# Optimization experiments

Hardware: AMD Instinct MI355X
Metric: run time of the kernel (lower is better)

Reference implementation:

```python
import jax, jax.numpy as jnp
import numpy as np

H = 16
D_MODEL = 1024
D_K = D_MODEL // H


def setup_inputs() -> dict:
    key = jax.random.key(0)
    ks = jax.random.split(key, 11)
    B, S, D = 2, 2048, D_MODEL
    sc = 1.0 / np.sqrt(D)
    return {
        "query": jax.random.normal(ks[0], (B, S, D), jnp.float32),
        "key": jax.random.normal(ks[1], (B, S, D), jnp.float32),
        "value": jax.random.normal(ks[2], (B, S, D), jnp.float32),
        "Wq": jax.random.normal(ks[3], (D, D), jnp.float32) * sc,
        "bq": jnp.zeros((D,), jnp.float32),
        "Wk": jax.random.normal(ks[4], (D, D), jnp.float32) * sc,
        "bk": jnp.zeros((D,), jnp.float32),
        "Wv": jax.random.normal(ks[5], (D, D), jnp.float32) * sc,
        "bv": jnp.zeros((D,), jnp.float32),
        "Wo": jax.random.normal(ks[6], (D, D), jnp.float32) * sc,
        "bo": jnp.zeros((D,), jnp.float32),
    }


def _split_heads(x, B, S):
    # [B,S,D] -> [B,H,S,d_k]
    return x.reshape(B, S, H, D_K).transpose(0, 2, 1, 3)


def reference(query, key, value, Wq, bq, Wk, bk, Wv, bv, Wo, bo):
    B, S, D = query.shape
    q = _split_heads(query @ Wq + bq, B, S)
    k = _split_heads(key @ Wk + bk, B, key.shape[1])
    v = _split_heads(value @ Wv + bv, B, value.shape[1])
    scores = jnp.einsum("bhqd,bhkd->bhqk", q, k) / jnp.sqrt(jnp.asarray(D_K, q.dtype))
    p_attn = jax.nn.softmax(scores, axis=-1)  # dropout is identity at inference
    x = jnp.einsum("bhqk,bhkd->bhqd", p_attn, v)
    x = x.transpose(0, 2, 1, 3).reshape(B, S, H * D_K)
    return x @ Wo + bo
```

## Files before the change

### kernel.cpp

```cpp
#include <hip/hip_runtime.h>

typedef unsigned short u16;
typedef unsigned int   u32;
typedef __bf16 bf16x8 __attribute__((ext_vector_type(8)));
typedef float  f32x4  __attribute__((ext_vector_type(4)));

__device__ __forceinline__ u16 f2bf(float f) {
  u32 u = __float_as_uint(f);
  u += 0x7fffu + ((u >> 16) & 1u);
  return (u16)(u >> 16);
}

__device__ __forceinline__ u32 cvt_pk_bf16(float a, float b) {
  u32 r;
  asm("v_cvt_pk_bf16_f32 %0, %1, %2" : "=v"(r) : "v"(a), "v"(b));
  return r;
}

__device__ __forceinline__ float max3f(float a, float b, float c) {
  float r;
  asm("v_max3_f32 %0, %1, %2, %3" : "=v"(r) : "v"(a), "v"(b), "v"(c));
  return r;
}

__device__ __forceinline__ void gll16(const void* g, void* l) {
  __builtin_amdgcn_global_load_lds(
      (__attribute__((address_space(1))) unsigned int*)(g),
      (__attribute__((address_space(3))) unsigned int*)(l), 16, 0, 0);
}

__device__ __forceinline__ int xcd_swz(int wg, int nwg) {
  int cpx = nwg >> 3;
  return (wg & 7) * cpx + (wg >> 3);
}

__device__ __forceinline__ void cvt8(const float* __restrict__ s, u16* __restrict__ d, int o) {
  float4 a = *(const float4*)(s + o);
  float4 b = *(const float4*)(s + o + 4);
  uint4 r;
  r.x = cvt_pk_bf16(a.x, a.y);
  r.y = cvt_pk_bf16(a.z, a.w);
  r.z = cvt_pk_bf16(b.x, b.y);
  r.w = cvt_pk_bf16(b.z, b.w);
  *(uint4*)(d + o) = r;
}

__global__ __launch_bounds__(256) void convert_in(
    const float* __restrict__ q, const float* __restrict__ k, const float* __restrict__ v,
    u16* __restrict__ qo, u16* __restrict__ ko, u16* __restrict__ vo) {
  int t = blockIdx.x * 256 + threadIdx.x;
  int o = t * 8;
  cvt8(q, qo, o);
  cvt8(k, ko, o);
  cvt8(v, vo, o);
}

__global__ __launch_bounds__(256) void convert_w(
    const float* __restrict__ Wq, const float* __restrict__ Wk,
    const float* __restrict__ Wv, const float* __restrict__ Wo,
    u16* __restrict__ Wqt, u16* __restrict__ Wkt,
    u16* __restrict__ Wvt, u16* __restrict__ Wot) {
  __shared__ __align__(16) u16 t[64][72];
  int z = blockIdx.z;
  const float* W = (z == 0) ? Wq : (z == 1) ? Wk : (z == 2) ? Wv : Wo;
  u16* Wt = (z == 0) ? Wqt : (z == 1) ? Wkt : (z == 2) ? Wvt : Wot;
  int k0 = blockIdx.y * 64, n0 = blockIdx.x * 64;
  int tid = threadIdx.x;
#pragma unroll
  for (int e = 0; e < 4; ++e) {
    int i = e * 256 + tid;
    int r = i >> 4, c4 = (i & 15) * 4;
    float4 vv = *(const float4*)(W + (size_t)(k0 + r) * 1024 + n0 + c4);
    union { u16 u[4]; uint2 w2; } p;
    p.u[0] = f2bf(vv.x); p.u[1] = f2bf(vv.y); p.u[2] = f2bf(vv.z); p.u[3] = f2bf(vv.w);
    *(uint2*)&t[r][c4] = p.w2;
  }
  __syncthreads();
#pragma unroll
  for (int e = 0; e < 2; ++e) {
    int i = e * 256 + tid;
    int rn = i >> 3, c8 = (i & 7) * 8;
    union { u16 u[8]; uint4 w4; } p;
#pragma unroll
    for (int kk = 0; kk < 8; ++kk) p.u[kk] = t[c8 + kk][rn];
    *(uint4*)(Wt + (size_t)(n0 + rn) * 1024 + k0 + c8) = p.w4;
  }
}

__device__ __forceinline__ void gemm_core(
    const u16* __restrict__ A,
    const u16* __restrict__ Bt,
    int K, int m0, int n0,
    u16* As, u16* Bs, f32x4 acc[4][4]) {
  const int tid = threadIdx.x;
  const int l = tid & 63;
  const int g = l >> 4, q16 = l & 15;
  const int wv = tid >> 6;
  const int wr = wv >> 1, wc = wv & 1;
#pragma unroll
  for (int mi = 0; mi < 4; ++mi)
#pragma unroll
    for (int ni = 0; ni < 4; ++ni) acc[mi][ni] = (f32x4){0.f, 0.f, 0.f, 0.f};

  for (int k0 = 0; k0 < K; k0 += 64) {
    __syncthreads();
#pragma unroll
    for (int c = 0; c < 4; ++c) {
      int i = c * 256 + tid;
      int row = i >> 3, ce = (i & 7) * 8;
      gll16(A + (size_t)(m0 + row) * K + k0 + ce, As + i * 8);
      gll16(Bt + (size_t)(n0 + row) * K + k0 + ce, Bs + i * 8);
    }
    __syncthreads();
#pragma unroll
    for (int kb = 0; kb < 2; ++kb) {
      bf16x8 af[4], bfr[4];
#pragma unroll
      for (int mi = 0; mi < 4; ++mi)
        af[mi] = *(const bf16x8*)(As + (wr * 64 + mi * 16 + q16) * 64 + kb * 32 + g * 8);
#pragma unroll
      for (int ni = 0; ni < 4; ++ni)
        bfr[ni] = *(const bf16x8*)(Bs + (wc * 64 + ni * 16 + q16) * 64 + kb * 32 + g * 8);
#pragma unroll
      for (int mi = 0; mi < 4; ++mi)
#pragma unroll
        for (int ni = 0; ni < 4; ++ni)
          acc[mi][ni] = __builtin_amdgcn_mfma_f32_16x16x32_bf16(af[mi], bfr[ni], acc[mi][ni], 0, 0, 0);
    }
  }
}

__global__ __launch_bounds__(256) void gemm_qkv(
    const u16* __restrict__ qA, const u16* __restrict__ kA, const u16* __restrict__ vA,
    const u16* __restrict__ qW, const u16* __restrict__ kW, const u16* __restrict__ vW,
    const float* __restrict__ qb, const float* __restrict__ kb2, const float* __restrict__ vb,
    u16* __restrict__ Qh, u16* __restrict__ Kh, u16* __restrict__ Vh, float qscale) {
  __shared__ __align__(16) u16 As[128 * 64];
  __shared__ __align__(16) u16 Bs[128 * 64];
  int z = blockIdx.z;
  const u16* A   = (z == 0) ? qA : (z == 1) ? kA : vA;
  const u16* Bt  = (z == 0) ? qW : (z == 1) ? kW : vW;
  const float* bias = (z == 0) ? qb : (z == 1) ? kb2 : vb;
  u16* out = (z == 0) ? Qh : (z == 1) ? Kh : Vh;
  float scale = (z == 0) ? qscale : 1.0f;
  int swz = xcd_swz(blockIdx.y * gridDim.x + blockIdx.x, gridDim.x * gridDim.y);
  int m0 = (swz >> 3) * 128, n0 = (swz & 7) * 128;
  f32x4 acc[4][4];
  gemm_core(A, Bt, 1024, m0, n0, As, Bs, acc);

  const int tid = threadIdx.x;
  const int l = tid & 63;
  const int g = l >> 4, q16 = l & 15;
  const int wv = tid >> 6;
  const int wr = wv >> 1, wc = wv & 1;
#pragma unroll
  for (int ni = 0; ni < 4; ++ni) {
    int n = n0 + wc * 64 + ni * 16 + q16;
    float bvv = bias[n];
    int hh = n >> 6, dk = n & 63;
#pragma unroll
    for (int mi = 0; mi < 4; ++mi) {
#pragma unroll
      for (int j = 0; j < 4; ++j) {
        int m = m0 + wr * 64 + mi * 16 + g * 4 + j;
        int b = m >> 11, s = m & 2047;
        float v = (acc[mi][ni][j] + bvv) * scale;
        out[(((size_t)b * 16 + hh) * 2048 + s) * 64 + dk] = f2bf(v);
      }
    }
  }
}

__global__ __launch_bounds__(256) void gemm_out(
    const u16* __restrict__ A, const u16* __restrict__ Bt,
    const float* __restrict__ bias, float* __restrict__ Out) {
  __shared__ __align__(16) u16 As[128 * 64];
  __shared__ __align__(16) u16 Bs[128 * 64];
  int swz = xcd_swz(blockIdx.y * gridDim.x + blockIdx.x, gridDim.x * gridDim.y);
  int m0 = (swz >> 3) * 128, n0 = (swz & 7) * 128;
  f32x4 acc[4][4];
  gemm_core(A, Bt, 1024, m0, n0, As, Bs, acc);

  const int tid = threadIdx.x;
  const int l = tid & 63;
  const int g = l >> 4, q16 = l & 15;
  const int wv = tid >> 6;
  const int wr = wv >> 1, wc = wv & 1;
#pragma unroll
  for (int ni = 0; ni < 4; ++ni) {
    int n = n0 + wc * 64 + ni * 16 + q16;
    float bvv = bias[n];
#pragma unroll
    for (int mi = 0; mi < 4; ++mi) {
#pragma unroll
      for (int j = 0; j < 4; ++j) {
        int m = m0 + wr * 64 + mi * 16 + g * 4 + j;
        Out[(size_t)m * 1024 + n] = acc[mi][ni][j] + bvv;
      }
    }
  }
}

__global__ __launch_bounds__(256) void transpose_v(const u16* __restrict__ Vh, u16* __restrict__ Vt) {
  __shared__ __align__(16) u16 t[64][72];
  int bh = blockIdx.y, s0 = blockIdx.x * 64;
  int tid = threadIdx.x;
#pragma unroll
  for (int e = 0; e < 2; ++e) {
    int i = e * 256 + tid;
    int r = i >> 3, c8 = (i & 7) * 8;
    uint4 vv = *(const uint4*)(Vh + ((size_t)bh * 2048 + s0 + r) * 64 + c8);
    *(uint4*)&t[r][c8] = vv;
  }
  __syncthreads();
#pragma unroll
  for (int e = 0; e < 2; ++e) {
    int i = e * 256 + tid;
    int d = i >> 3, s8 = (i & 7) * 8;
    union { u16 u[8]; uint4 w4; } p;
#pragma unroll
    for (int kk = 0; kk < 8; ++kk) p.u[kk] = t[s8 + kk][d];
    *(uint4*)(Vt + ((size_t)bh * 64 + d) * 2048 + s0 + s8) = p.w4;
  }
}

__global__ __launch_bounds__(256, 3) void attn_kernel(
    const u16* __restrict__ Qh,
    const u16* __restrict__ Kh,
    const u16* __restrict__ Vt,
    u16* __restrict__ Xb) {
  __shared__ __align__(16) u16 Ks[2][64 * 64];
  __shared__ __align__(16) u16 Vs[2][64 * 64];
  __shared__ __align__(16) u16 Ps[4][16][72];

  const int tid = threadIdx.x;
  const int l = tid & 63, wv = tid >> 6;
  const int g = l >> 4, q16 = l & 15;
  int swz = xcd_swz(blockIdx.y * gridDim.x + blockIdx.x, gridDim.x * gridDim.y);
  const int qblk = swz & 31, bh = swz >> 5;
  const int b = bh >> 4, h = bh & 15;
  const int qrow0 = qblk * 64 + wv * 16;

  const u16* Kbase = Kh + (size_t)bh * 2048 * 64;
  const u16* Vbase = Vt + (size_t)bh * 64 * 2048;

  bf16x8 bq[2];
#pragma unroll
  for (int kb = 0; kb < 2; ++kb)
    bq[kb] = *(const bf16x8*)(Qh + ((size_t)bh * 2048 + qrow0 + q16) * 64 + kb * 32 + g * 8);

  f32x4 x[4];
#pragma unroll
  for (int ni = 0; ni < 4; ++ni) x[ni] = (f32x4){0.f, 0.f, 0.f, 0.f};
  float m_run = -3e38f, l_run = 0.f;

#pragma unroll
  for (int c = 0; c < 2; ++c) {
    int i = c * 256 + tid;
    int row = i >> 3, sc8 = (i & 7) ^ (row & 7);
    gll16(Kbase + (size_t)row * 64 + sc8 * 8, &Ks[0][i * 8]);
    gll16(Vbase + (size_t)row * 2048 + sc8 * 8, &Vs[0][i * 8]);
  }
  asm volatile("s_waitcnt vmcnt(0)" ::: "memory");
  __builtin_amdgcn_s_barrier();

  for (int kt = 0; kt < 32; ++kt) {
    const int cb = kt & 1, nb = cb ^ 1;
    if (kt + 1 < 32) {
#pragma unroll
      for (int c = 0; c < 2; ++c) {
        int i = c * 256 + tid;
        int row = i >> 3, sc8 = (i & 7) ^ (row & 7);
        gll16(Kbase + ((size_t)(kt + 1) * 64 + row) * 64 + sc8 * 8, &Ks[nb][i * 8]);
        gll16(Vbase + (size_t)row * 2048 + (kt + 1) * 64 + sc8 * 8, &Vs[nb][i * 8]);
      }
    }

    f32x4 st[4];
#pragma unroll
    for (int mi = 0; mi < 4; ++mi) st[mi] = (f32x4){0.f, 0.f, 0.f, 0.f};
    __builtin_amdgcn_s_setprio(1);
#pragma unroll
    for (int mi = 0; mi < 4; ++mi) {
      int row = mi * 16 + q16;
#pragma unroll
      for (int kb = 0; kb < 2; ++kb) {
        int pc8 = (kb * 4 + g) ^ (row & 7);
        bf16x8 ak = *(const bf16x8*)(&Ks[cb][row * 64 + pc8 * 8]);
        st[mi] = __builtin_amdgcn_mfma_f32_16x16x32_bf16(ak, bq[kb], st[mi], 0, 0, 0);
      }
    }
    __builtin_amdgcn_s_setprio(0);

    float ma = max3f(st[0][0], st[0][1], st[0][2]);
    ma = max3f(ma, st[0][3], st[1][0]);
    ma = max3f(ma, st[1][1], st[1][2]);
    ma = fmaxf(ma, st[1][3]);
    float mb = max3f(st[2][0], st[2][1], st[2][2]);
    mb = max3f(mb, st[2][3], st[3][0]);
    mb = max3f(mb, st[3][1], st[3][2]);
    mb = fmaxf(mb, st[3][3]);
    float mx = fmaxf(ma, mb);
    mx = fmaxf(mx, __shfl_xor(mx, 16));
    mx = fmaxf(mx, __shfl_xor(mx, 32));

    float mref, sf;
    if (__all(mx <= m_run + 8.f)) {
      mref = m_run; sf = 1.f;
    } else {
      mref = fmaxf(m_run, mx);
      sf = __builtin_amdgcn_exp2f(m_run - mref);
      m_run = mref;
#pragma unroll
      for (int j = 0; j < 4; ++j) {
        float sfx = __shfl(sf, g * 4 + j);
#pragma unroll
        for (int ni = 0; ni < 4; ++ni) x[ni][j] *= sfx;
      }
    }

    float rs = 0.f;
#pragma unroll
    for (int mi = 0; mi < 4; ++mi)
#pragma unroll
      for (int j = 0; j < 4; ++j) {
        float p = __builtin_amdgcn_exp2f(st[mi][j] - mref);
        st[mi][j] = p;
        rs += p;
      }
    rs += __shfl_xor(rs, 16);
    rs += __shfl_xor(rs, 32);
    l_run = l_run * sf + rs;

#pragma unroll
    for (int mi = 0; mi < 4; ++mi) {
      uint2 w;
      w.x = cvt_pk_bf16(st[mi][0], st[mi][1]);
      w.y = cvt_pk_bf16(st[mi][2], st[mi][3]);
      *(uint2*)&Ps[wv][q16][mi * 16 + g * 4] = w;
    }

    __builtin_amdgcn_s_setprio(1);
#pragma unroll
    for (int kkb = 0; kkb < 2; ++kkb) {
      bf16x8 ap = *(const bf16x8*)&Ps[wv][q16][kkb * 32 + g * 8];
#pragma unroll
      for (int ni = 0; ni < 4; ++ni) {
        int d = ni * 16 + q16;
        int pc8 = (kkb * 4 + g) ^ (d & 7);
        bf16x8 vf = *(const bf16x8*)(&Vs[cb][d * 64 + pc8 * 8]);
        x[ni] = __builtin_amdgcn_mfma_f32_16x16x32_bf16(ap, vf, x[ni], 0, 0, 0);
      }
    }
    __builtin_amdgcn_s_setprio(0);

    asm volatile("s_waitcnt vmcnt(0)" ::: "memory");
    __builtin_amdgcn_s_barrier();
  }

  float li = 1.0f / l_run;
#pragma unroll
  for (int j = 0; j < 4; ++j) {
    float lv = __shfl(li, g * 4 + j);
    int srw = b * 2048 + qblk * 64 + wv * 16 + g * 4 + j;
#pragma unroll
    for (int ni = 0; ni < 4; ++ni) {
      int col = h * 64 + ni * 16 + q16;
      Xb[(size_t)srw * 1024 + col] = f2bf(x[ni][j] * lv);
    }
  }
}

extern "C" void kernel_launch(void* const* d_in, const int* in_sizes, int n_in,
                              void* d_out, int out_size, void* d_ws, size_t ws_size,
                              hipStream_t stream) {
  (void)in_sizes; (void)n_in; (void)out_size; (void)ws_size;
  const float* q  = (const float*)d_in[0];
  const float* k  = (const float*)d_in[1];
  const float* v  = (const float*)d_in[2];
  const float* Wq = (const float*)d_in[3];
  const float* bq = (const float*)d_in[4];
  const float* Wk = (const float*)d_in[5];
  const float* bk = (const float*)d_in[6];
  const float* Wv = (const float*)d_in[7];
  const float* bv = (const float*)d_in[8];
  const float* Wo = (const float*)d_in[9];
  const float* bo = (const float*)d_in[10];

  char* W = (char*)d_ws;
  const size_t MB = 1ull << 20;
  u16* qbf = (u16*)(W + 0 * MB);
  u16* kbf = (u16*)(W + 8 * MB);
  u16* vbf = (u16*)(W + 16 * MB);
  u16* wqt = (u16*)(W + 24 * MB);
  u16* wkt = (u16*)(W + 26 * MB);
  u16* wvt = (u16*)(W + 28 * MB);
  u16* wot = (u16*)(W + 30 * MB);
  u16* Qh  = (u16*)(W + 32 * MB);
  u16* Kh  = (u16*)(W + 40 * MB);
  u16* Vh  = (u16*)(W + 48 * MB);
  u16* Vtb = (u16*)(W + 56 * MB);
  u16* Xb  = (u16*)(W + 64 * MB);

  convert_in<<<2048, 256, 0, stream>>>(q, k, v, qbf, kbf, vbf);
  convert_w<<<dim3(16, 16, 4), 256, 0, stream>>>(Wq, Wk, Wv, Wo, wqt, wkt, wvt, wot);
  const float QSCALE = 0.125f * 1.4426950408889634f;
  gemm_qkv<<<dim3(8, 32, 3), 256, 0, stream>>>(qbf, kbf, vbf, wqt, wkt, wvt,
                                               bq, bk, bv, Qh, Kh, Vh, QSCALE);
  transpose_v<<<dim3(32, 32), 256, 0, stream>>>(Vh, Vtb);
  attn_kernel<<<dim3(32, 32), 256, 0, stream>>>(Qh, Kh, Vtb, Xb);
  gemm_out<<<dim3(8, 32), 256, 0, stream>>>(Xb, wot, bo, (float*)d_out);
}
```

Before: 177.9 us.

## Use 128-query attention blocks with 8 waves and triple-buffered K/V prefetch

The attention kernel now uses 512-thread blocks, each covering 128 query rows with 8 waves, so every K/V tile loaded into shared memory serves twice as many queries. K/V staging moves from double to triple buffering with a two-tile-ahead prefetch and a partial vmcnt wait, so loads overlap more compute. The s_setprio hints around the MFMA sections are removed. The costs are a grid of half as many blocks, more shared memory per block, and lower occupancy control, since the launch bound changes from (256,3) to (512).

```diff
diff --git a/kernel.cpp b/kernel.cpp
--- a/kernel.cpp
+++ b/kernel.cpp
@@ -224,23 +224,25 @@
   }
 }
 
-__global__ __launch_bounds__(256, 3) void attn_kernel(
+__global__ __launch_bounds__(512) void attn_kernel(
     const u16* __restrict__ Qh,
     const u16* __restrict__ Kh,
     const u16* __restrict__ Vt,
     u16* __restrict__ Xb) {
-  __shared__ __align__(16) u16 Ks[2][64 * 64];
-  __shared__ __align__(16) u16 Vs[2][64 * 64];
-  __shared__ __align__(16) u16 Ps[4][16][72];
+  __shared__ __align__(16) u16 Ks[3][64 * 64];
+  __shared__ __align__(16) u16 Vs[3][64 * 64];
+  __shared__ __align__(16) u16 Ps[8][16][72];
 
   const int tid = threadIdx.x;
   const int l = tid & 63, wv = tid >> 6;
   const int g = l >> 4, q16 = l & 15;
-  int swz = xcd_swz(blockIdx.y * gridDim.x + blockIdx.x, gridDim.x * gridDim.y);
-  const int qblk = swz & 31, bh = swz >> 5;
+  const int swz = xcd_swz(blockIdx.y * gridDim.x + blockIdx.x, gridDim.x * gridDim.y);
+  const int qblk = swz & 15, bh = swz >> 4;
   const int b = bh >> 4, h = bh & 15;
-  const int qrow0 = qblk * 64 + wv * 16;
-
+  const int qrow0 = qblk * 128 + wv * 16;
+
+  const int srow = tid >> 3;
+  const int sc8  = (tid & 7) ^ (srow & 7);
   const u16* Kbase = Kh + (size_t)bh * 2048 * 64;
   const u16* Vbase = Vt + (size_t)bh * 64 * 2048;
 
@@ -254,32 +256,24 @@
   for (int ni = 0; ni < 4; ++ni) x[ni] = (f32x4){0.f, 0.f, 0.f, 0.f};
   float m_run = -3e38f, l_run = 0.f;
 
-#pragma unroll
-  for (int c = 0; c < 2; ++c) {
-    int i = c * 256 + tid;
-    int row = i >> 3, sc8 = (i & 7) ^ (row & 7);
-    gll16(Kbase + (size_t)row * 64 + sc8 * 8, &Ks[0][i * 8]);
-    gll16(Vbase + (size_t)row * 2048 + sc8 * 8, &Vs[0][i * 8]);
-  }
-  asm volatile("s_waitcnt vmcnt(0)" ::: "memory");
+  gll16(Kbase + (size_t)srow * 64 + sc8 * 8, &Ks[0][tid * 8]);
+  gll16(Vbase + (size_t)srow * 2048 + sc8 * 8, &Vs[0][tid * 8]);
+  gll16(Kbase + ((size_t)64 + srow) * 64 + sc8 * 8, &Ks[1][tid * 8]);
+  gll16(Vbase + (size_t)srow * 2048 + 64 + sc8 * 8, &Vs[1][tid * 8]);
+  asm volatile("s_waitcnt vmcnt(2)" ::: "memory");
   __builtin_amdgcn_s_barrier();
 
   for (int kt = 0; kt < 32; ++kt) {
-    const int cb = kt & 1, nb = cb ^ 1;
-    if (kt + 1 < 32) {
-#pragma unroll
-      for (int c = 0; c < 2; ++c) {
-        int i = c * 256 + tid;
-        int row = i >> 3, sc8 = (i & 7) ^ (row & 7);
-        gll16(Kbase + ((size_t)(kt + 1) * 64 + row) * 64 + sc8 * 8, &Ks[nb][i * 8]);
-        gll16(Vbase + (size_t)row * 2048 + (kt + 1) * 64 + sc8 * 8, &Vs[nb][i * 8]);
-      }
+    const int cb = kt % 3;
+    if (kt + 2 < 32) {
+      const int pb = (kt + 2) % 3;
+      gll16(Kbase + ((size_t)(kt + 2) * 64 + srow) * 64 + sc8 * 8, &Ks[pb][tid * 8]);
+      gll16(Vbase + (size_t)srow * 2048 + (kt + 2) * 64 + sc8 * 8, &Vs[pb][tid * 8]);
     }
 
     f32x4 st[4];
 #pragma unroll
     for (int mi = 0; mi < 4; ++mi) st[mi] = (f32x4){0.f, 0.f, 0.f, 0.f};
-    __builtin_amdgcn_s_setprio(1);
 #pragma unroll
     for (int mi = 0; mi < 4; ++mi) {
       int row = mi * 16 + q16;
@@ -290,7 +284,6 @@
         st[mi] = __builtin_amdgcn_mfma_f32_16x16x32_bf16(ak, bq[kb], st[mi], 0, 0, 0);
       }
     }
-    __builtin_amdgcn_s_setprio(0);
 
     float ma = max3f(st[0][0], st[0][1], st[0][2]);
     ma = max3f(ma, st[0][3], st[1][0]);
@@ -340,7 +333,6 @@
       *(uint2*)&Ps[wv][q16][mi * 16 + g * 4] = w;
     }
 
-    __builtin_amdgcn_s_setprio(1);
 #pragma unroll
     for (int kkb = 0; kkb < 2; ++kkb) {
       bf16x8 ap = *(const bf16x8*)&Ps[wv][q16][kkb * 32 + g * 8];
@@ -352,9 +344,12 @@
         x[ni] = __builtin_amdgcn_mfma_f32_16x16x32_bf16(ap, vf, x[ni], 0, 0, 0);
       }
     }
-    __builtin_amdgcn_s_setprio(0);
-
-    asm volatile("s_waitcnt vmcnt(0)" ::: "memory");
+
+    if (kt < 30) {
+      asm volatile("s_waitcnt vmcnt(2)" ::: "memory");
+    } else {
+      asm volatile("s_waitcnt vmcnt(0)" ::: "memory");
+    }
     __builtin_amdgcn_s_barrier();
   }
 
@@ -362,7 +357,7 @@
 #pragma unroll
   for (int j = 0; j < 4; ++j) {
     float lv = __shfl(li, g * 4 + j);
-    int srw = b * 2048 + qblk * 64 + wv * 16 + g * 4 + j;
+    int srw = b * 2048 + qblk * 128 + wv * 16 + g * 4 + j;
 #pragma unroll
     for (int ni = 0; ni < 4; ++ni) {
       int col = h * 64 + ni * 16 + q16;
@@ -408,6 +403,6 @@
   gemm_qkv<<<dim3(8, 32, 3), 256, 0, stream>>>(qbf, kbf, vbf, wqt, wkt, wvt,
                                                bq, bk, bv, Qh, Kh, Vh, QSCALE);
   transpose_v<<<dim3(32, 32), 256, 0, stream>>>(Vh, Vtb);
-  attn_kernel<<<dim3(32, 32), 256, 0, stream>>>(Qh, Kh, Vtb, Xb);
+  attn_kernel<<<dim3(16, 32), 512, 0, stream>>>(Qh, Kh, Vtb, Xb);
   gemm_out<<<dim3(8, 32), 256, 0, stream>>>(Xb, wot, bo, (float*)d_out);
 }
```

Result: faster. 152.2 us (-14.4%).
